# Optimization experiments

Hardware: AMD Instinct MI355X
Metric: run time of the kernel (lower is better)

## Reference

```python
import jax, jax.numpy as jnp
import numpy as np

B, L, D, H, DK, DV = 512, 256, 1024, 16, 64, 64
TEMP = float(np.sqrt(D))  # source uses sqrt(d_model), not sqrt(d_k)
LN_EPS = 1.0              # LayerNormalization default eps=1, added to std


def setup_inputs() -> dict:
    key = jax.random.key(0)
    ks = jax.random.split(key, 7)
    u = lambda k, shape: jax.random.uniform(k, shape, jnp.float32, -0.04, 0.04)
    return {
        "q": jax.random.normal(ks[0], (B, D), jnp.float32),
        "k": jax.random.normal(ks[1], (B, L, D), jnp.float32),
        "v": jax.random.normal(ks[2], (B, L, D), jnp.float32),
        "Wq": u(ks[3], (H, DK, D)),   # stacked per-head q-proj weights
        "Wk": u(ks[4], (H, DK, D)),
        "Wv": u(ks[5], (H, DV, D)),
        "Wp": u(ks[6], (D, H * DV)),  # output projection (nn.Linear weight layout)
        "scale": jnp.ones((D,), jnp.float32),
        "offset": jnp.zeros((D,), jnp.float32),
    }


def reference(q, k, v, Wq, Wk, Wv, Wp, scale, offset):
    # per-head projections (batched over heads instead of a Python loop)
    hq = jnp.einsum('bd,hkd->bhk', q, Wq)       # [B,H,DK]
    hk = jnp.einsum('bld,hkd->bhlk', k, Wk)     # [B,H,L,DK]
    hv = jnp.einsum('bld,hvd->bhlv', v, Wv)     # [B,H,L,DV]
    # single-query dot-product attention per head
    scores = jnp.einsum('bhk,bhlk->bhl', hq, hk) / TEMP
    w = jax.nn.softmax(scores, axis=-1)         # dropout is identity (rate 0 / eval)
    ctx = jnp.einsum('bhl,bhlv->bhv', w, hv).reshape(B, H * DV)
    # output projection + residual
    out = ctx @ Wp.T + q
    # LayerNormalization: unbiased std (torch.std default), eps added to std
    mean = out.mean(axis=-1, keepdims=True)
    std = jnp.sqrt(jnp.sum((out - mean) ** 2, axis=-1, keepdims=True) / (D - 1))
    return scale * (out - mean) / (std + LN_EPS) + offset
```

## Files before the change

kernel.cpp:

```cpp
#include <hip/hip_runtime.h>

#define B_ 512
#define L_ 256
#define D_ 1024
#define H_ 16
#define DK_ 64
#define DV_ 64

typedef float f32x4 __attribute__((ext_vector_type(4)));
typedef float f32x2 __attribute__((ext_vector_type(2)));
typedef __bf16 bf16x8 __attribute__((ext_vector_type(8)));
typedef __bf16 bf16x2 __attribute__((ext_vector_type(2)));

#define MFMA16(a, b, c) __builtin_amdgcn_mfma_f32_16x16x32_bf16((a), (b), (c), 0, 0, 0)

__device__ inline bf16x8 cvt8(f32x4 a, f32x4 b) {
  bf16x8 r;
  r[0] = (__bf16)a[0]; r[1] = (__bf16)a[1]; r[2] = (__bf16)a[2]; r[3] = (__bf16)a[3];
  r[4] = (__bf16)b[0]; r[5] = (__bf16)b[1]; r[6] = (__bf16)b[2]; r[7] = (__bf16)b[3];
  return r;
}

__global__ __launch_bounds__(256) void k_hq(const float* __restrict__ q,
                                            const float* __restrict__ Wq,
                                            __bf16* __restrict__ hq) {
  int tid = threadIdx.x, lane = tid & 63, wid = tid >> 6;
  int r16 = lane & 15, g = lane >> 4;
  int n0 = (blockIdx.x * 4 + wid) * 16;
  int m0 = blockIdx.y * 16;
  const float* arow = q  + (size_t)(m0 + r16) * D_;
  const float* brow = Wq + (size_t)(n0 + r16) * D_;
  f32x4 acc = {0.f, 0.f, 0.f, 0.f};
  for (int ks = 0; ks < D_ / 32; ++ks) {
    int k0 = ks * 32 + g * 8;
    f32x4 a0 = *(const f32x4*)(arow + k0);
    f32x4 a1 = *(const f32x4*)(arow + k0 + 4);
    f32x4 b0 = *(const f32x4*)(brow + k0);
    f32x4 b1 = *(const f32x4*)(brow + k0 + 4);
    acc = MFMA16(cvt8(a0, a1), cvt8(b0, b1), acc);
  }
#pragma unroll
  for (int r = 0; r < 4; ++r) {
    int m = m0 + g * 4 + r;
    hq[(size_t)m * (H_ * DK_) + n0 + r16] = (__bf16)acc[r];
  }
}

__global__ __launch_bounds__(256) void k_aq(const __bf16* __restrict__ hq,
                                            const float* __restrict__ Wk,
                                            __bf16* __restrict__ Aq) {
  int tid = threadIdx.x, lane = tid & 63, wid = tid >> 6;
  int r16 = lane & 15, g = lane >> 4;
  int h = blockIdx.z;
  int n0 = (blockIdx.x * 4 + wid) * 16;
  int m0 = blockIdx.y * 16;
  const __bf16* arow = hq + (size_t)(m0 + r16) * (H_ * DK_) + h * DK_;
  const float* bcol = Wk + (size_t)h * DK_ * D_ + n0 + r16;
  f32x4 acc = {0.f, 0.f, 0.f, 0.f};
#pragma unroll
  for (int ks = 0; ks < 2; ++ks) {
    int k0 = ks * 32 + g * 8;
    bf16x8 a = *(const bf16x8*)(arow + k0);
    f32x4 c0, c1;
#pragma unroll
    for (int j = 0; j < 4; ++j) c0[j] = bcol[(size_t)(k0 + j) * D_];
#pragma unroll
    for (int j = 0; j < 4; ++j) c1[j] = bcol[(size_t)(k0 + 4 + j) * D_];
    acc = MFMA16(a, cvt8(c0, c1), acc);
  }
#pragma unroll
  for (int r = 0; r < 4; ++r) {
    int m = m0 + g * 4 + r;
    Aq[(size_t)m * (H_ * D_) + (size_t)h * D_ + n0 + r16] = (__bf16)acc[r];
  }
}

__global__ __launch_bounds__(256) void k_score(const float* __restrict__ kg,
                                               const __bf16* __restrict__ Aq,
                                               float* __restrict__ sc) {
  int tid = threadIdx.x, lane = tid & 63, wv = tid >> 6;
  int r16 = lane & 15, g = lane >> 4;
  int b = blockIdx.y;
  int l0 = blockIdx.x * 64 + wv * 16;
  const __bf16* AqB = Aq + (size_t)b * H_ * D_;
  const float*  kR  = kg + ((size_t)b * L_ + l0 + r16) * D_;
  f32x4 acc = {0.f, 0.f, 0.f, 0.f};
#pragma unroll 4
  for (int ks = 0; ks < D_ / 32; ++ks) {
    int k0 = ks * 32 + g * 8;
    bf16x8 a = *(const bf16x8*)(AqB + (size_t)r16 * D_ + k0);
    f32x4 b0 = *(const f32x4*)(kR + k0);
    f32x4 b1 = *(const f32x4*)(kR + k0 + 4);
    acc = MFMA16(a, cvt8(b0, b1), acc);
  }
#pragma unroll
  for (int r = 0; r < 4; ++r) {
    int h = g * 4 + r;
    sc[((size_t)b * H_ + h) * L_ + l0 + r16] = acc[r] * 0.03125f;
  }
}

#define WPAD 20
__global__ __launch_bounds__(256) void k_cv(const float* __restrict__ vg,
                                            const float* __restrict__ sc,
                                            __bf16* __restrict__ cv) {
  __shared__ float wT[L_][WPAD];

  int tid = threadIdx.x, lane = tid & 63, wv = tid >> 6;
  int b = blockIdx.y;

  const float* scB = sc + (size_t)b * H_ * L_;
#pragma unroll
  for (int rr = 0; rr < 4; ++rr) {
    int row = wv * 4 + rr;
    const float* srow = scB + (size_t)row * L_;
    float x0 = srow[lane], x1 = srow[lane + 64];
    float x2 = srow[lane + 128], x3 = srow[lane + 192];
    float m = fmaxf(fmaxf(x0, x1), fmaxf(x2, x3));
#pragma unroll
    for (int off = 32; off; off >>= 1) m = fmaxf(m, __shfl_xor(m, off));
    float e0 = __expf(x0 - m), e1 = __expf(x1 - m);
    float e2 = __expf(x2 - m), e3 = __expf(x3 - m);
    float s = e0 + e1 + e2 + e3;
#pragma unroll
    for (int off = 32; off; off >>= 1) s += __shfl_xor(s, off);
    float inv = 1.0f / s;
    wT[lane]      [row] = e0 * inv;
    wT[lane + 64] [row] = e1 * inv;
    wT[lane + 128][row] = e2 * inv;
    wT[lane + 192][row] = e3 * inv;
  }
  __syncthreads();

  int c0 = blockIdx.x * 512 + tid * 2;
  const float* vB = vg + (size_t)b * L_ * D_ + c0;
  f32x2 acc[16];
#pragma unroll
  for (int h = 0; h < 16; ++h) acc[h] = (f32x2){0.f, 0.f};

#pragma unroll 2
  for (int l = 0; l < L_; ++l) {
    f32x2 v2 = *(const f32x2*)(vB + (size_t)l * D_);
    f32x4 w0 = *(const f32x4*)(&wT[l][0]);
    f32x4 w1 = *(const f32x4*)(&wT[l][4]);
    f32x4 w2 = *(const f32x4*)(&wT[l][8]);
    f32x4 w3 = *(const f32x4*)(&wT[l][12]);
#pragma unroll
    for (int j = 0; j < 4; ++j) {
      acc[j]      += w0[j] * v2;
      acc[4 + j]  += w1[j] * v2;
      acc[8 + j]  += w2[j] * v2;
      acc[12 + j] += w3[j] * v2;
    }
  }
#pragma unroll
  for (int h = 0; h < 16; ++h) {
    bf16x2 o;
    o[0] = (__bf16)acc[h][0];
    o[1] = (__bf16)acc[h][1];
    *(bf16x2*)(cv + ((size_t)b * H_ + h) * D_ + c0) = o;
  }
}

__global__ __launch_bounds__(256) void k_ctx(const __bf16* __restrict__ cv,
                                             const float* __restrict__ Wv,
                                             __bf16* __restrict__ ctx) {
  int tid = threadIdx.x, lane = tid & 63, wid = tid >> 6;
  int r16 = lane & 15, g = lane >> 4;
  int h = blockIdx.z, m0 = blockIdx.y * 16, n0 = wid * 16;
  const __bf16* arow = cv + (size_t)(m0 + r16) * (H_ * D_) + (size_t)h * D_;
  const float* brow = Wv + (size_t)h * DV_ * D_ + (size_t)(n0 + r16) * D_;
  f32x4 acc = {0.f, 0.f, 0.f, 0.f};
  for (int ks = 0; ks < D_ / 32; ++ks) {
    int k0 = ks * 32 + g * 8;
    bf16x8 a = *(const bf16x8*)(arow + k0);
    f32x4 b0 = *(const f32x4*)(brow + k0);
    f32x4 b1 = *(const f32x4*)(brow + k0 + 4);
    acc = MFMA16(a, cvt8(b0, b1), acc);
  }
#pragma unroll
  for (int r = 0; r < 4; ++r) {
    int m = m0 + g * 4 + r;
    ctx[(size_t)m * (H_ * DV_) + h * DV_ + n0 + r16] = (__bf16)acc[r];
  }
}

__global__ __launch_bounds__(256) void k_out(const __bf16* __restrict__ ctx,
                                             const float* __restrict__ Wp,
                                             const float* __restrict__ q,
                                             float* __restrict__ outp) {
  int tid = threadIdx.x, lane = tid & 63, wid = tid >> 6;
  int r16 = lane & 15, g = lane >> 4;
  int n0 = (blockIdx.x * 4 + wid) * 16;
  int m0 = blockIdx.y * 16;
  const __bf16* arow = ctx + (size_t)(m0 + r16) * D_;
  const float* brow = Wp + (size_t)(n0 + r16) * D_;
  f32x4 acc = {0.f, 0.f, 0.f, 0.f};
  for (int ks = 0; ks < D_ / 32; ++ks) {
    int k0 = ks * 32 + g * 8;
    bf16x8 a = *(const bf16x8*)(arow + k0);
    f32x4 b0 = *(const f32x4*)(brow + k0);
    f32x4 b1 = *(const f32x4*)(brow + k0 + 4);
    acc = MFMA16(a, cvt8(b0, b1), acc);
  }
#pragma unroll
  for (int r = 0; r < 4; ++r) {
    int m = m0 + g * 4 + r;
    outp[(size_t)m * D_ + n0 + r16] = acc[r] + q[(size_t)m * D_ + n0 + r16];
  }
}

__global__ __launch_bounds__(256) void k_ln(const float* __restrict__ xin,
                                            const float* __restrict__ scale,
                                            const float* __restrict__ offs,
                                            float* __restrict__ out) {
  __shared__ float red[4];
  int b = blockIdx.x, tid = threadIdx.x;
  const float* row = xin + (size_t)b * D_;
  f32x4 x = *(const f32x4*)(row + tid * 4);
  float s = x[0] + x[1] + x[2] + x[3];
#pragma unroll
  for (int off = 32; off; off >>= 1) s += __shfl_xor(s, off);
  if ((tid & 63) == 0) red[tid >> 6] = s;
  __syncthreads();
  float mean = (red[0] + red[1] + red[2] + red[3]) * (1.0f / D_);
  __syncthreads();
  float vs = 0.f;
#pragma unroll
  for (int j = 0; j < 4; ++j) { float d = x[j] - mean; vs += d * d; }
#pragma unroll
  for (int off = 32; off; off >>= 1) vs += __shfl_xor(vs, off);
  if ((tid & 63) == 0) red[tid >> 6] = vs;
  __syncthreads();
  float var = (red[0] + red[1] + red[2] + red[3]) * (1.0f / (D_ - 1));
  float inv = 1.0f / (sqrtf(var) + 1.0f);
  f32x4 sc = *(const f32x4*)(scale + tid * 4);
  f32x4 of = *(const f32x4*)(offs + tid * 4);
  f32x4 o;
#pragma unroll
  for (int j = 0; j < 4; ++j) o[j] = sc[j] * (x[j] - mean) * inv + of[j];
  *(f32x4*)(out + (size_t)b * D_ + tid * 4) = o;
}

extern "C" void kernel_launch(void* const* d_in, const int* in_sizes, int n_in,
                              void* d_out, int out_size, void* d_ws, size_t ws_size,
                              hipStream_t stream) {
  const float* q     = (const float*)d_in[0];
  const float* k     = (const float*)d_in[1];
  const float* v     = (const float*)d_in[2];
  const float* Wq    = (const float*)d_in[3];
  const float* Wk    = (const float*)d_in[4];
  const float* Wv    = (const float*)d_in[5];
  const float* Wp    = (const float*)d_in[6];
  const float* scale = (const float*)d_in[7];
  const float* offs  = (const float*)d_in[8];
  float* out = (float*)d_out;

  char* ws = (char*)d_ws;
  __bf16* hq   = (__bf16*)(ws);
  __bf16* Aq   = (__bf16*)(ws + (size_t)1  * (1 << 20));
  float*  scr  = (float*) (ws + (size_t)17 * (1 << 20));
  __bf16* cv   = (__bf16*)(ws + (size_t)25 * (1 << 20));
  __bf16* ctx  = (__bf16*)(ws + (size_t)41 * (1 << 20));
  float*  outp = (float*) (ws + (size_t)42 * (1 << 20));

  k_hq   <<<dim3(16, 32),     256, 0, stream>>>(q, Wq, hq);
  k_aq   <<<dim3(16, 32, 16), 256, 0, stream>>>(hq, Wk, Aq);
  k_score<<<dim3(4, 512),     256, 0, stream>>>(k, Aq, scr);
  k_cv   <<<dim3(2, 512),     256, 0, stream>>>(v, scr, cv);
  k_ctx  <<<dim3(1, 32, 16),  256, 0, stream>>>(cv, Wv, ctx);
  k_out  <<<dim3(16, 32),     256, 0, stream>>>(ctx, Wp, q, outp);
  k_ln   <<<dim3(512),        256, 0, stream>>>(outp, scale, offs, out);
}
```

Measured before the change: 317.6 us.

## Fuse score and softmax-weighted V kernels into one per-batch attention kernel

Merges the score GEMM and the softmax/weighted-V accumulation into a single kernel with one 512-thread block per batch. Scores now stay in LDS instead of going through a global scratch buffer, and the 1/32 temperature is folded into the Aq projection. This removes one launch and the score write/read round trip. In exchange the grid shrinks from 2048 and 1024 blocks to 512 larger blocks, so occupancy and latency hiding on the K and V streams may drop.

```diff
diff --git a/kernel.cpp b/kernel.cpp
--- a/kernel.cpp
+++ b/kernel.cpp
@@ -71,51 +71,49 @@
 #pragma unroll
   for (int r = 0; r < 4; ++r) {
     int m = m0 + g * 4 + r;
-    Aq[(size_t)m * (H_ * D_) + (size_t)h * D_ + n0 + r16] = (__bf16)acc[r];
-  }
-}
-
-__global__ __launch_bounds__(256) void k_score(const float* __restrict__ kg,
+    Aq[(size_t)m * (H_ * D_) + (size_t)h * D_ + n0 + r16] = (__bf16)(acc[r] * 0.03125f);
+  }
+}
+
+#define WPAD 20
+__global__ __launch_bounds__(512) void k_attn2(const float* __restrict__ kg,
+                                               const float* __restrict__ vg,
                                                const __bf16* __restrict__ Aq,
-                                               float* __restrict__ sc) {
+                                               __bf16* __restrict__ cv) {
+  __shared__ float s_lds[H_][L_ + 4];
+  __shared__ float wT[L_][WPAD];
+
+  int b = blockIdx.x;
   int tid = threadIdx.x, lane = tid & 63, wv = tid >> 6;
   int r16 = lane & 15, g = lane >> 4;
-  int b = blockIdx.y;
-  int l0 = blockIdx.x * 64 + wv * 16;
   const __bf16* AqB = Aq + (size_t)b * H_ * D_;
-  const float*  kR  = kg + ((size_t)b * L_ + l0 + r16) * D_;
-  f32x4 acc = {0.f, 0.f, 0.f, 0.f};
+  const float*  kB  = kg + (size_t)b * L_ * D_;
+  const float*  vB  = vg + (size_t)b * L_ * D_;
+
+  f32x4 accA[2] = {{0.f,0.f,0.f,0.f}, {0.f,0.f,0.f,0.f}};
+  const float* kR0 = kB + (size_t)(wv * 32 + r16) * D_;
+  const float* kR1 = kB + (size_t)(wv * 32 + 16 + r16) * D_;
 #pragma unroll 4
   for (int ks = 0; ks < D_ / 32; ++ks) {
     int k0 = ks * 32 + g * 8;
     bf16x8 a = *(const bf16x8*)(AqB + (size_t)r16 * D_ + k0);
-    f32x4 b0 = *(const f32x4*)(kR + k0);
-    f32x4 b1 = *(const f32x4*)(kR + k0 + 4);
-    acc = MFMA16(a, cvt8(b0, b1), acc);
-  }
-#pragma unroll
-  for (int r = 0; r < 4; ++r) {
-    int h = g * 4 + r;
-    sc[((size_t)b * H_ + h) * L_ + l0 + r16] = acc[r] * 0.03125f;
-  }
-}
-
-#define WPAD 20
-__global__ __launch_bounds__(256) void k_cv(const float* __restrict__ vg,
-                                            const float* __restrict__ sc,
-                                            __bf16* __restrict__ cv) {
-  __shared__ float wT[L_][WPAD];
-
-  int tid = threadIdx.x, lane = tid & 63, wv = tid >> 6;
-  int b = blockIdx.y;
-
-  const float* scB = sc + (size_t)b * H_ * L_;
-#pragma unroll
-  for (int rr = 0; rr < 4; ++rr) {
-    int row = wv * 4 + rr;
-    const float* srow = scB + (size_t)row * L_;
-    float x0 = srow[lane], x1 = srow[lane + 64];
-    float x2 = srow[lane + 128], x3 = srow[lane + 192];
+    accA[0] = MFMA16(a, cvt8(*(const f32x4*)(kR0 + k0), *(const f32x4*)(kR0 + k0 + 4)), accA[0]);
+    accA[1] = MFMA16(a, cvt8(*(const f32x4*)(kR1 + k0), *(const f32x4*)(kR1 + k0 + 4)), accA[1]);
+  }
+#pragma unroll
+  for (int nt = 0; nt < 2; ++nt)
+#pragma unroll
+    for (int r = 0; r < 4; ++r)
+      s_lds[g * 4 + r][wv * 32 + nt * 16 + r16] = accA[nt][r];
+  __syncthreads();
+
+#pragma unroll
+  for (int rr = 0; rr < 2; ++rr) {
+    int row = wv * 2 + rr;
+    float x0 = s_lds[row][lane];
+    float x1 = s_lds[row][lane + 64];
+    float x2 = s_lds[row][lane + 128];
+    float x3 = s_lds[row][lane + 192];
     float m = fmaxf(fmaxf(x0, x1), fmaxf(x2, x3));
 #pragma unroll
     for (int off = 32; off; off >>= 1) m = fmaxf(m, __shfl_xor(m, off));
@@ -132,15 +130,15 @@
   }
   __syncthreads();
 
-  int c0 = blockIdx.x * 512 + tid * 2;
-  const float* vB = vg + (size_t)b * L_ * D_ + c0;
+  int c0 = tid * 2;
+  const float* vC = vB + c0;
   f32x2 acc[16];
 #pragma unroll
   for (int h = 0; h < 16; ++h) acc[h] = (f32x2){0.f, 0.f};
 
 #pragma unroll 2
   for (int l = 0; l < L_; ++l) {
-    f32x2 v2 = *(const f32x2*)(vB + (size_t)l * D_);
+    f32x2 v2 = *(const f32x2*)(vC + (size_t)l * D_);
     f32x4 w0 = *(const f32x4*)(&wT[l][0]);
     f32x4 w1 = *(const f32x4*)(&wT[l][4]);
     f32x4 w2 = *(const f32x4*)(&wT[l][8]);
@@ -259,15 +257,13 @@
   char* ws = (char*)d_ws;
   __bf16* hq   = (__bf16*)(ws);
   __bf16* Aq   = (__bf16*)(ws + (size_t)1  * (1 << 20));
-  float*  scr  = (float*) (ws + (size_t)17 * (1 << 20));
-  __bf16* cv   = (__bf16*)(ws + (size_t)25 * (1 << 20));
-  __bf16* ctx  = (__bf16*)(ws + (size_t)41 * (1 << 20));
-  float*  outp = (float*) (ws + (size_t)42 * (1 << 20));
+  __bf16* cv   = (__bf16*)(ws + (size_t)17 * (1 << 20));
+  __bf16* ctx  = (__bf16*)(ws + (size_t)33 * (1 << 20));
+  float*  outp = (float*) (ws + (size_t)34 * (1 << 20));
 
   k_hq   <<<dim3(16, 32),     256, 0, stream>>>(q, Wq, hq);
   k_aq   <<<dim3(16, 32, 16), 256, 0, stream>>>(hq, Wk, Aq);
-  k_score<<<dim3(4, 512),     256, 0, stream>>>(k, Aq, scr);
-  k_cv   <<<dim3(2, 512),     256, 0, stream>>>(v, scr, cv);
+  k_attn2<<<dim3(512),        512, 0, stream>>>(k, v, Aq, cv);
   k_ctx  <<<dim3(1, 32, 16),  256, 0, stream>>>(cv, Wv, ctx);
   k_out  <<<dim3(16, 32),     256, 0, stream>>>(ctx, Wp, q, outp);
   k_ln   <<<dim3(512),        256, 0, stream>>>(outp, scale, offs, out);
```

Result: slower. 335.6 us (+5.7%).

## Pre-transpose Wk for coalesced loads, fold score scale, widen k_cv grid

Applied to the files above, without the earlier changes.

Adds a transpose kernel that writes Wk as [H,D,DK] so k_aq can use contiguous vector loads in place of strided column gathers. The 1/32 score scale moves from k_score into k_aq's Aq output, which changes where the bf16 rounding happens. k_cv now processes one column per thread over a doubled grid (4x512 blocks) for more parallelism, and its shared-memory pad drops to 17, which may misalign the f32x4 LDS reads. The cost is an extra kernel launch and workspace buffer.

```diff
diff --git a/kernel.cpp b/kernel.cpp
--- a/kernel.cpp
+++ b/kernel.cpp
@@ -21,6 +21,28 @@
   return r;
 }
 
+__global__ __launch_bounds__(256) void k_wkT(const float* __restrict__ Wk,
+                                             float* __restrict__ WkT) {
+  __shared__ float t[64][65];
+  int h = blockIdx.y, d0 = blockIdx.x * 64;
+  int tid = threadIdx.x;
+  int lr = tid >> 6;
+  int lc = tid & 63;
+  const float* src = Wk + (size_t)h * DK_ * D_;
+#pragma unroll
+  for (int r = 0; r < 16; ++r) {
+    int kk = r * 4 + lr;
+    t[kk][lc] = src[(size_t)kk * D_ + d0 + lc];
+  }
+  __syncthreads();
+  float* dst = WkT + (size_t)h * D_ * DK_;
+#pragma unroll
+  for (int r = 0; r < 16; ++r) {
+    int d = r * 4 + lr;
+    dst[(size_t)(d0 + d) * DK_ + lc] = t[lc][d];
+  }
+}
+
 __global__ __launch_bounds__(256) void k_hq(const float* __restrict__ q,
                                             const float* __restrict__ Wq,
                                             __bf16* __restrict__ hq) {
@@ -47,7 +69,7 @@
 }
 
 __global__ __launch_bounds__(256) void k_aq(const __bf16* __restrict__ hq,
-                                            const float* __restrict__ Wk,
+                                            const float* __restrict__ WkT,
                                             __bf16* __restrict__ Aq) {
   int tid = threadIdx.x, lane = tid & 63, wid = tid >> 6;
   int r16 = lane & 15, g = lane >> 4;
@@ -55,23 +77,20 @@
   int n0 = (blockIdx.x * 4 + wid) * 16;
   int m0 = blockIdx.y * 16;
   const __bf16* arow = hq + (size_t)(m0 + r16) * (H_ * DK_) + h * DK_;
-  const float* bcol = Wk + (size_t)h * DK_ * D_ + n0 + r16;
+  const float* brow = WkT + ((size_t)h * D_ + n0 + r16) * DK_;
   f32x4 acc = {0.f, 0.f, 0.f, 0.f};
 #pragma unroll
   for (int ks = 0; ks < 2; ++ks) {
     int k0 = ks * 32 + g * 8;
     bf16x8 a = *(const bf16x8*)(arow + k0);
-    f32x4 c0, c1;
-#pragma unroll
-    for (int j = 0; j < 4; ++j) c0[j] = bcol[(size_t)(k0 + j) * D_];
-#pragma unroll
-    for (int j = 0; j < 4; ++j) c1[j] = bcol[(size_t)(k0 + 4 + j) * D_];
-    acc = MFMA16(a, cvt8(c0, c1), acc);
-  }
-#pragma unroll
-  for (int r = 0; r < 4; ++r) {
-    int m = m0 + g * 4 + r;
-    Aq[(size_t)m * (H_ * D_) + (size_t)h * D_ + n0 + r16] = (__bf16)acc[r];
+    f32x4 b0 = *(const f32x4*)(brow + k0);
+    f32x4 b1 = *(const f32x4*)(brow + k0 + 4);
+    acc = MFMA16(a, cvt8(b0, b1), acc);
+  }
+#pragma unroll
+  for (int r = 0; r < 4; ++r) {
+    int m = m0 + g * 4 + r;
+    Aq[(size_t)m * (H_ * D_) + (size_t)h * D_ + n0 + r16] = (__bf16)(acc[r] * 0.03125f);
   }
 }
 
@@ -96,11 +115,11 @@
 #pragma unroll
   for (int r = 0; r < 4; ++r) {
     int h = g * 4 + r;
-    sc[((size_t)b * H_ + h) * L_ + l0 + r16] = acc[r] * 0.03125f;
-  }
-}
-
-#define WPAD 20
+    sc[((size_t)b * H_ + h) * L_ + l0 + r16] = acc[r];
+  }
+}
+
+#define WPAD 17
 __global__ __launch_bounds__(256) void k_cv(const float* __restrict__ vg,
                                             const float* __restrict__ sc,
                                             __bf16* __restrict__ cv) {
@@ -132,34 +151,30 @@
   }
   __syncthreads();
 
-  int c0 = blockIdx.x * 512 + tid * 2;
-  const float* vB = vg + (size_t)b * L_ * D_ + c0;
-  f32x2 acc[16];
-#pragma unroll
-  for (int h = 0; h < 16; ++h) acc[h] = (f32x2){0.f, 0.f};
+  int c0 = blockIdx.x * 256 + tid;
+  const float* vC = vg + (size_t)b * L_ * D_ + c0;
+  float acc[16];
+#pragma unroll
+  for (int h = 0; h < 16; ++h) acc[h] = 0.f;
 
 #pragma unroll 2
   for (int l = 0; l < L_; ++l) {
-    f32x2 v2 = *(const f32x2*)(vB + (size_t)l * D_);
+    float v1 = vC[(size_t)l * D_];
     f32x4 w0 = *(const f32x4*)(&wT[l][0]);
     f32x4 w1 = *(const f32x4*)(&wT[l][4]);
     f32x4 w2 = *(const f32x4*)(&wT[l][8]);
     f32x4 w3 = *(const f32x4*)(&wT[l][12]);
 #pragma unroll
     for (int j = 0; j < 4; ++j) {
-      acc[j]      += w0[j] * v2;
-      acc[4 + j]  += w1[j] * v2;
-      acc[8 + j]  += w2[j] * v2;
-      acc[12 + j] += w3[j] * v2;
+      acc[j]      += w0[j] * v1;
+      acc[4 + j]  += w1[j] * v1;
+      acc[8 + j]  += w2[j] * v1;
+      acc[12 + j] += w3[j] * v1;
     }
   }
 #pragma unroll
-  for (int h = 0; h < 16; ++h) {
-    bf16x2 o;
-    o[0] = (__bf16)acc[h][0];
-    o[1] = (__bf16)acc[h][1];
-    *(bf16x2*)(cv + ((size_t)b * H_ + h) * D_ + c0) = o;
-  }
+  for (int h = 0; h < 16; ++h)
+    cv[((size_t)b * H_ + h) * D_ + c0] = (__bf16)acc[h];
 }
 
 __global__ __launch_bounds__(256) void k_ctx(const __bf16* __restrict__ cv,
@@ -263,11 +278,13 @@
   __bf16* cv   = (__bf16*)(ws + (size_t)25 * (1 << 20));
   __bf16* ctx  = (__bf16*)(ws + (size_t)41 * (1 << 20));
   float*  outp = (float*) (ws + (size_t)42 * (1 << 20));
-
+  float*  WkT  = (float*) (ws + (size_t)44 * (1 << 20));
+
+  k_wkT  <<<dim3(16, 16),     256, 0, stream>>>(Wk, WkT);
   k_hq   <<<dim3(16, 32),     256, 0, stream>>>(q, Wq, hq);
-  k_aq   <<<dim3(16, 32, 16), 256, 0, stream>>>(hq, Wk, Aq);
+  k_aq   <<<dim3(16, 32, 16), 256, 0, stream>>>(hq, WkT, Aq);
   k_score<<<dim3(4, 512),     256, 0, stream>>>(k, Aq, scr);
-  k_cv   <<<dim3(2, 512),     256, 0, stream>>>(v, scr, cv);
+  k_cv   <<<dim3(4, 512),     256, 0, stream>>>(v, scr, cv);
   k_ctx  <<<dim3(1, 32, 16),  256, 0, stream>>>(cv, Wv, ctx);
   k_out  <<<dim3(16, 32),     256, 0, stream>>>(ctx, Wp, q, outp);
   k_ln   <<<dim3(512),        256, 0, stream>>>(outp, scale, offs, out);
```

After: 375.7 us. +18.3%, slower.

## Compute weighted V sum with bf16 MFMA instead of scalar FP32 FMAs

Applied to the files above, without the earlier changes.

Rewrites k_cv so the softmax-weights-by-V product runs on bf16 16x16x32 MFMA tiles. The softmax weights are stored in LDS as bf16 in [H][L] layout, and V columns are loaded strided and converted to bf16. The 1/32 temperature scale moves from the score output into the Aq precompute, and the grid is widened to 4 column blocks. This removes the scalar FP32 FMA loop, at the cost of bf16 rounding of the weights and V, and strided per-row V loads that may coalesce less well.

```diff
diff --git a/kernel.cpp b/kernel.cpp
--- a/kernel.cpp
+++ b/kernel.cpp
@@ -71,7 +71,7 @@
 #pragma unroll
   for (int r = 0; r < 4; ++r) {
     int m = m0 + g * 4 + r;
-    Aq[(size_t)m * (H_ * D_) + (size_t)h * D_ + n0 + r16] = (__bf16)acc[r];
+    Aq[(size_t)m * (H_ * D_) + (size_t)h * D_ + n0 + r16] = (__bf16)(acc[r] * 0.03125f);
   }
 }
 
@@ -96,17 +96,17 @@
 #pragma unroll
   for (int r = 0; r < 4; ++r) {
     int h = g * 4 + r;
-    sc[((size_t)b * H_ + h) * L_ + l0 + r16] = acc[r] * 0.03125f;
-  }
-}
-
-#define WPAD 20
+    sc[((size_t)b * H_ + h) * L_ + l0 + r16] = acc[r];
+  }
+}
+
 __global__ __launch_bounds__(256) void k_cv(const float* __restrict__ vg,
                                             const float* __restrict__ sc,
                                             __bf16* __restrict__ cv) {
-  __shared__ float wT[L_][WPAD];
+  __shared__ __bf16 wA[H_][L_ + 8];
 
   int tid = threadIdx.x, lane = tid & 63, wv = tid >> 6;
+  int r16 = lane & 15, g = (lane >> 4) & 3;
   int b = blockIdx.y;
 
   const float* scB = sc + (size_t)b * H_ * L_;
@@ -125,41 +125,37 @@
 #pragma unroll
     for (int off = 32; off; off >>= 1) s += __shfl_xor(s, off);
     float inv = 1.0f / s;
-    wT[lane]      [row] = e0 * inv;
-    wT[lane + 64] [row] = e1 * inv;
-    wT[lane + 128][row] = e2 * inv;
-    wT[lane + 192][row] = e3 * inv;
-  }
-  __syncthreads();
-
-  int c0 = blockIdx.x * 512 + tid * 2;
-  const float* vB = vg + (size_t)b * L_ * D_ + c0;
-  f32x2 acc[16];
-#pragma unroll
-  for (int h = 0; h < 16; ++h) acc[h] = (f32x2){0.f, 0.f};
-
-#pragma unroll 2
-  for (int l = 0; l < L_; ++l) {
-    f32x2 v2 = *(const f32x2*)(vB + (size_t)l * D_);
-    f32x4 w0 = *(const f32x4*)(&wT[l][0]);
-    f32x4 w1 = *(const f32x4*)(&wT[l][4]);
-    f32x4 w2 = *(const f32x4*)(&wT[l][8]);
-    f32x4 w3 = *(const f32x4*)(&wT[l][12]);
-#pragma unroll
-    for (int j = 0; j < 4; ++j) {
-      acc[j]      += w0[j] * v2;
-      acc[4 + j]  += w1[j] * v2;
-      acc[8 + j]  += w2[j] * v2;
-      acc[12 + j] += w3[j] * v2;
+    wA[row][lane]       = (__bf16)(e0 * inv);
+    wA[row][lane + 64]  = (__bf16)(e1 * inv);
+    wA[row][lane + 128] = (__bf16)(e2 * inv);
+    wA[row][lane + 192] = (__bf16)(e3 * inv);
+  }
+  __syncthreads();
+
+  int dbase = blockIdx.x * 256 + wv * 64;
+  const float* vB = vg + (size_t)b * L_ * D_ + dbase;
+  f32x4 acc[4] = {{0.f,0.f,0.f,0.f},{0.f,0.f,0.f,0.f},
+                  {0.f,0.f,0.f,0.f},{0.f,0.f,0.f,0.f}};
+  for (int ks = 0; ks < 8; ++ks) {
+    int l0 = ks * 32 + g * 8;
+    bf16x8 a = *(const bf16x8*)(&wA[r16][l0]);
+    const float* pv = vB + (size_t)l0 * D_ + r16;
+#pragma unroll
+    for (int nt = 0; nt < 4; ++nt) {
+      const float* p = pv + nt * 16;
+      f32x4 c0, c1;
+#pragma unroll
+      for (int j = 0; j < 4; ++j) c0[j] = p[(size_t)j * D_];
+#pragma unroll
+      for (int j = 0; j < 4; ++j) c1[j] = p[(size_t)(4 + j) * D_];
+      acc[nt] = MFMA16(a, cvt8(c0, c1), acc[nt]);
     }
   }
 #pragma unroll
-  for (int h = 0; h < 16; ++h) {
-    bf16x2 o;
-    o[0] = (__bf16)acc[h][0];
-    o[1] = (__bf16)acc[h][1];
-    *(bf16x2*)(cv + ((size_t)b * H_ + h) * D_ + c0) = o;
-  }
+  for (int nt = 0; nt < 4; ++nt)
+#pragma unroll
+    for (int r = 0; r < 4; ++r)
+      cv[((size_t)b * H_ + g * 4 + r) * D_ + dbase + nt * 16 + r16] = (__bf16)acc[nt][r];
 }
 
 __global__ __launch_bounds__(256) void k_ctx(const __bf16* __restrict__ cv,
@@ -267,7 +263,7 @@
   k_hq   <<<dim3(16, 32),     256, 0, stream>>>(q, Wq, hq);
   k_aq   <<<dim3(16, 32, 16), 256, 0, stream>>>(hq, Wk, Aq);
   k_score<<<dim3(4, 512),     256, 0, stream>>>(k, Aq, scr);
-  k_cv   <<<dim3(2, 512),     256, 0, stream>>>(v, scr, cv);
+  k_cv   <<<dim3(4, 512),     256, 0, stream>>>(v, scr, cv);
   k_ctx  <<<dim3(1, 32, 16),  256, 0, stream>>>(cv, Wv, ctx);
   k_out  <<<dim3(16, 32),     256, 0, stream>>>(ctx, Wp, q, outp);
   k_ln   <<<dim3(512),        256, 0, stream>>>(outp, scale, offs, out);
```

Measured after the change: 312.9 us. About the same (-1.5%).
